# Kernel optimization log

Measured on AMD Instinct MI355X. Metric: run time of the kernel, lower is better.

## Reference

```python
import jax, jax.numpy as jnp
import numpy as np
import math

B, N, DIM, H = 4, 2048, 1024, 16
DH = DIM // H

def setup_inputs() -> dict:
    key = jax.random.key(0)
    ks = jax.random.split(key, 7)
    return {
        "x": jax.random.normal(ks[0], (B, N, DIM), dtype=jnp.float32),
        "qkv_w": jax.random.normal(ks[1], (3 * DIM, DIM), dtype=jnp.float32) * 0.02,
        "qkv_b": jax.random.normal(ks[2], (3 * DIM,), dtype=jnp.float32) * 0.02,
        "proj_w": jax.random.normal(ks[3], (DIM, DIM), dtype=jnp.float32) * 0.02,
        "proj_b": jax.random.normal(ks[4], (DIM,), dtype=jnp.float32) * 0.02,
        "temperature": jnp.ones((1,), dtype=jnp.float32) * 0.1,
        "eps": jax.random.normal(ks[5], (B, H, N, DH), dtype=jnp.float32),
    }

def reference(x, qkv_w, qkv_b, proj_w, proj_b, temperature, eps):
    b, n, dim = x.shape
    qkv = x @ qkv_w.T + qkv_b
    qkv = qkv.reshape(b, n, 3, H, DH).transpose(2, 0, 3, 1, 4)
    q, k, v = qkv[0], qkv[1], qkv[2]
    # quantum fluctuation: additive gaussian noise on q, scaled by sigmoid(temperature)
    q = q + eps * jax.nn.sigmoid(temperature)
    scale = 1.0 / math.sqrt(DH)
    attn = jnp.einsum("bhqd,bhkd->bhqk", q, k) * scale  # [B,H,N,N]
    attn = jax.nn.softmax(attn, axis=-1)
    out = jnp.einsum("bhqk,bhkd->bhqd", attn, v)  # [B,H,N,DH]
    out = out.transpose(0, 2, 1, 3).reshape(b, n, dim)
    return out @ proj_w.T + proj_b
```

## Files before the change

kernel.cpp:

```cpp
#include <hip/hip_runtime.h>
#include <math.h>

#define B_   4
#define N_   2048
#define DIM_ 1024
#define H_   16
#define DH_  64
#define M_   (B_ * N_)
#define QKV_ELEMS ((size_t)B_ * H_ * N_ * DH_)

typedef __attribute__((ext_vector_type(8))) short short8;
typedef __attribute__((ext_vector_type(4))) float floatx4;

static __device__ inline unsigned short f2bf(float f) {
    union { float f; unsigned u; } v; v.f = f;
    unsigned r = (v.u + 0x7fffu + ((v.u >> 16) & 1u)) >> 16;
    return (unsigned short)r;
}

static __device__ inline void async_copy16(const void* g, void* l) {
    __builtin_amdgcn_global_load_lds(
        (const __attribute__((address_space(1))) unsigned int*)g,
        (__attribute__((address_space(3))) unsigned int*)l, 16, 0, 0);
}

__global__ __launch_bounds__(256) void f32_to_bf16_kernel(
    const float* __restrict__ src, unsigned short* __restrict__ dst, int n8)
{
    int i = blockIdx.x * 256 + threadIdx.x;
    if (i >= n8) return;
    float4 a = ((const float4*)src)[i * 2];
    float4 b = ((const float4*)src)[i * 2 + 1];
    short8 o;
    o[0] = f2bf(a.x); o[1] = f2bf(a.y); o[2] = f2bf(a.z); o[3] = f2bf(a.w);
    o[4] = f2bf(b.x); o[5] = f2bf(b.y); o[6] = f2bf(b.z); o[7] = f2bf(b.w);
    *(short8*)(dst + (size_t)i * 8) = o;
}

#define GEMM_BODY(Aptr, Bptr, K)                                               \
    __shared__ unsigned short As[128 * 32];                                    \
    __shared__ unsigned short Bs[128 * 32];                                    \
    const int tid  = threadIdx.x;                                              \
    const int lane = tid & 63;                                                 \
    const int wv   = tid >> 6;                                                 \
    const int l15  = lane & 15, quad = lane >> 4;                              \
    const int wrow = (wv >> 1) * 64, wcol = (wv & 1) * 64;                     \
    const int m0 = blockIdx.y * 128, n0 = blockIdx.x * 128;                    \
    const int lrow = lane >> 2;                                                \
    const int lkc  = (lane & 3) * 8;                                           \
    const unsigned short* ga0 = Aptr + (size_t)(m0 + wv * 32 + lrow) * K + lkc;\
    const unsigned short* ga1 = ga0 + (size_t)16 * K;                          \
    const unsigned short* gb0 = Bptr + (size_t)(n0 + wv * 32 + lrow) * K + lkc;\
    const unsigned short* gb1 = gb0 + (size_t)16 * K;                          \
    unsigned short* lA0 = &As[wv * 1024];                                      \
    unsigned short* lA1 = lA0 + 512;                                           \
    unsigned short* lB0 = &Bs[wv * 1024];                                      \
    unsigned short* lB1 = lB0 + 512;                                           \
    floatx4 acc[4][4] = {};                                                    \
    for (int k0 = 0; k0 < K; k0 += 32) {                                       \
        __syncthreads();                                                       \
        async_copy16(ga0 + k0, lA0);                                           \
        async_copy16(ga1 + k0, lA1);                                           \
        async_copy16(gb0 + k0, lB0);                                           \
        async_copy16(gb1 + k0, lB1);                                           \
        __syncthreads();                                                       \
        short8 af[4], bf[4];                                                   \
        _Pragma("unroll")                                                      \
        for (int mt = 0; mt < 4; ++mt)                                         \
            af[mt] = *(const short8*)&As[(wrow + mt * 16 + l15) * 32 + quad * 8];\
        _Pragma("unroll")                                                      \
        for (int nt = 0; nt < 4; ++nt)                                         \
            bf[nt] = *(const short8*)&Bs[(wcol + nt * 16 + l15) * 32 + quad * 8];\
        _Pragma("unroll")                                                      \
        for (int mt = 0; mt < 4; ++mt)                                         \
            _Pragma("unroll")                                                  \
            for (int nt = 0; nt < 4; ++nt)                                     \
                acc[mt][nt] = __builtin_amdgcn_mfma_f32_16x16x32_bf16(         \
                    af[mt], bf[nt], acc[mt][nt], 0, 0, 0);                     \
    }

__global__ __launch_bounds__(256) void gemm_qkv_bf16(
    const unsigned short* __restrict__ A, const unsigned short* __restrict__ Bm,
    const float* __restrict__ bias, const float* __restrict__ eps,
    const float* __restrict__ temp,
    unsigned short* __restrict__ qb, unsigned short* __restrict__ kb,
    unsigned short* __restrict__ vb)
{
    GEMM_BODY(A, Bm, 1024)

    const float sig = 1.0f / (1.0f + __expf(-temp[0]));
    const float qscale = 0.125f * 1.44269504f;
#pragma unroll
    for (int mt = 0; mt < 4; ++mt) {
#pragma unroll
        for (int r = 0; r < 4; ++r) {
            const int m  = m0 + wrow + mt * 16 + quad * 4 + r;
            const int b  = m >> 11;
            const int nn = m & 2047;
#pragma unroll
            for (int nt = 0; nt < 4; ++nt) {
                const int n = n0 + wcol + nt * 16 + l15;
                float val = acc[mt][nt][r] + bias[n];
                const int which = n >> 10;
                const int d  = n & 1023;
                const int h  = d >> 6;
                const int dd = d & 63;
                const size_t bh = (size_t)(b * H_ + h);
                if (which == 0) {
                    const size_t idx = (bh * N_ + nn) * DH_ + dd;
                    qb[idx] = f2bf((val + eps[idx] * sig) * qscale);
                } else if (which == 1) {
                    kb[(bh * N_ + nn) * DH_ + dd] = f2bf(val);
                } else {
                    vb[(bh * DH_ + dd) * N_ + nn] = f2bf(val);
                }
            }
        }
    }
}

__global__ __launch_bounds__(256) void gemm_proj_bf16(
    const unsigned short* __restrict__ A, const unsigned short* __restrict__ Bm,
    const float* __restrict__ bias, float* __restrict__ out)
{
    GEMM_BODY(A, Bm, 1024)

#pragma unroll
    for (int mt = 0; mt < 4; ++mt) {
#pragma unroll
        for (int r = 0; r < 4; ++r) {
            const int m = m0 + wrow + mt * 16 + quad * 4 + r;
#pragma unroll
            for (int nt = 0; nt < 4; ++nt) {
                const int n = n0 + wcol + nt * 16 + l15;
                out[(size_t)m * 1024 + n] = acc[mt][nt][r] + bias[n];
            }
        }
    }
}

__global__ __launch_bounds__(256) void attn_kernel(
    const unsigned short* __restrict__ qb, const unsigned short* __restrict__ kb,
    const unsigned short* __restrict__ vt, unsigned short* __restrict__ attn_out)
{
    __shared__ unsigned short Ks[64 * 72];
    __shared__ unsigned short Vs[64 * 72];
    __shared__ unsigned short Ps[64 * 72];

    const int tid  = threadIdx.x;
    const int lane = tid & 63;
    const int wv   = tid >> 6;
    const int l15  = lane & 15;
    const int quad = lane >> 4;

    const int bh = blockIdx.y;
    const int b  = bh >> 4, h = bh & 15;
    const int q0 = blockIdx.x * 64;
    const int qr = q0 + wv * 16;

    const unsigned short* qp = qb + ((size_t)bh * N_ + qr + l15) * DH_;
    const short8 qf0 = *(const short8*)(qp + quad * 8);
    const short8 qf1 = *(const short8*)(qp + 32 + quad * 8);

    floatx4 o[4] = {};
    float l_acc[4] = {0.f, 0.f, 0.f, 0.f};

    const unsigned short* kb_bh = kb + (size_t)bh * N_ * DH_;
    const unsigned short* vt_bh = vt + (size_t)bh * DH_ * N_;

    for (int kt = 0; kt < 32; ++kt) {
        const unsigned short* kbase = kb_bh + (size_t)kt * 64 * DH_;
        const unsigned short* vbase = vt_bh + kt * 64;

        __syncthreads();
#pragma unroll
        for (int c = tid; c < 512; c += 256) {
            int r = c >> 3, off = (c & 7) << 3;
            *(short8*)&Ks[r * 72 + off] = *(const short8*)(kbase + r * 64 + off);
            *(short8*)&Vs[r * 72 + off] = *(const short8*)(vbase + (size_t)r * N_ + off);
        }
        __syncthreads();

        floatx4 s[4];
#pragma unroll
        for (int nt = 0; nt < 4; ++nt) {
            const unsigned short* krow = &Ks[(nt * 16 + l15) * 72];
            short8 kf0 = *(const short8*)(krow + quad * 8);
            short8 kf1 = *(const short8*)(krow + 32 + quad * 8);
            floatx4 c = {};
            c = __builtin_amdgcn_mfma_f32_16x16x32_bf16(qf0, kf0, c, 0, 0, 0);
            c = __builtin_amdgcn_mfma_f32_16x16x32_bf16(qf1, kf1, c, 0, 0, 0);
            s[nt] = c;
        }

#pragma unroll
        for (int nt = 0; nt < 4; ++nt)
#pragma unroll
            for (int r = 0; r < 4; ++r)
                s[nt][r] = __builtin_amdgcn_exp2f(s[nt][r]);
#pragma unroll
        for (int r = 0; r < 4; ++r)
            l_acc[r] += (s[0][r] + s[1][r]) + (s[2][r] + s[3][r]);

#pragma unroll
        for (int nt = 0; nt < 4; ++nt)
#pragma unroll
            for (int r = 0; r < 4; ++r) {
                unsigned u = (__float_as_uint(s[nt][r]) + 0x8000u) >> 16;
                Ps[(wv * 16 + quad * 4 + r) * 72 + nt * 16 + l15] = (unsigned short)u;
            }

        const unsigned short* prow = &Ps[(wv * 16 + l15) * 72];
        short8 pf0 = *(const short8*)(prow + quad * 8);
        short8 pf1 = *(const short8*)(prow + 32 + quad * 8);

#pragma unroll
        for (int dt = 0; dt < 4; ++dt) {
            const unsigned short* vrow = &Vs[(dt * 16 + l15) * 72];
            short8 vf0 = *(const short8*)(vrow + quad * 8);
            short8 vf1 = *(const short8*)(vrow + 32 + quad * 8);
            o[dt] = __builtin_amdgcn_mfma_f32_16x16x32_bf16(pf0, vf0, o[dt], 0, 0, 0);
            o[dt] = __builtin_amdgcn_mfma_f32_16x16x32_bf16(pf1, vf1, o[dt], 0, 0, 0);
        }
    }

    float inv[4];
#pragma unroll
    for (int r = 0; r < 4; ++r) {
        float l = l_acc[r];
#pragma unroll
        for (int off = 1; off < 16; off <<= 1)
            l += __shfl_xor(l, off, 64);
        inv[r] = 1.0f / l;
    }

#pragma unroll
    for (int dt = 0; dt < 4; ++dt) {
#pragma unroll
        for (int r = 0; r < 4; ++r) {
            int m = qr + quad * 4 + r;
            attn_out[((size_t)b * N_ + m) * DIM_ + h * DH_ + dt * 16 + l15] =
                f2bf(o[dt][r] * inv[r]);
        }
    }
}

extern "C" void kernel_launch(void* const* d_in, const int* in_sizes, int n_in,
                              void* d_out, int out_size, void* d_ws, size_t ws_size,
                              hipStream_t stream) {
    const float* x      = (const float*)d_in[0];
    const float* qkv_w  = (const float*)d_in[1];
    const float* qkv_b  = (const float*)d_in[2];
    const float* proj_w = (const float*)d_in[3];
    const float* proj_b = (const float*)d_in[4];
    const float* temp   = (const float*)d_in[5];
    const float* eps    = (const float*)d_in[6];
    float* out = (float*)d_out;

    unsigned short* qb   = (unsigned short*)d_ws;
    unsigned short* kb   = qb + QKV_ELEMS;
    unsigned short* vb   = kb + QKV_ELEMS;
    unsigned short* xb   = vb + QKV_ELEMS;
    unsigned short* wqb  = xb + QKV_ELEMS;
    unsigned short* pwb  = wqb + (size_t)3 * DIM_ * DIM_;
    unsigned short* attn = pwb + (size_t)DIM_ * DIM_;

    dim3 blk(256);
    f32_to_bf16_kernel<<<dim3(8388608 / 8 / 256), blk, 0, stream>>>(x, xb, 8388608 / 8);
    f32_to_bf16_kernel<<<dim3(3145728 / 8 / 256), blk, 0, stream>>>(qkv_w, wqb, 3145728 / 8);
    f32_to_bf16_kernel<<<dim3(1048576 / 8 / 256), blk, 0, stream>>>(proj_w, pwb, 1048576 / 8);

    gemm_qkv_bf16<<<dim3(24, 64), blk, 0, stream>>>(xb, wqb, qkv_b, eps, temp,
                                                    qb, kb, vb);
    attn_kernel<<<dim3(32, 64), blk, 0, stream>>>(qb, kb, vb, attn);
    gemm_proj_bf16<<<dim3(8, 64), blk, 0, stream>>>(attn, pwb, proj_b, out);
}
```

Baseline: 390.5 us.

## Restructure attention kernel with async double-buffered K/V, swizzled LDS, 2-wave blocks

Rewrites the attention kernel to use 128-thread blocks where each wave handles 32 query rows, with K/V tiles of 32 keys loaded via async global-to-LDS copies into double buffers so the next tile loads during compute. LDS layouts use XOR swizzles instead of padding, S is computed transposed (K as A operand) so P can be packed and written as bf16 pairs, and s_setprio brackets the MFMA sections. Block indices are remapped so that neighbouring blocks in launch order work on different heads, which is meant to change L2 locality. The aim is to hide global load latency and cut LDS traffic and syncs, at the cost of more registers per wave and more complex indexing.

```diff
diff --git a/kernel.cpp b/kernel.cpp
--- a/kernel.cpp
+++ b/kernel.cpp
@@ -139,108 +139,134 @@
     }
 }
 
-__global__ __launch_bounds__(256) void attn_kernel(
+__global__ __launch_bounds__(128) void attn_kernel(
     const unsigned short* __restrict__ qb, const unsigned short* __restrict__ kb,
     const unsigned short* __restrict__ vt, unsigned short* __restrict__ attn_out)
 {
-    __shared__ unsigned short Ks[64 * 72];
-    __shared__ unsigned short Vs[64 * 72];
-    __shared__ unsigned short Ps[64 * 72];
+    __shared__ unsigned short Ks[2][32 * 64];
+    __shared__ unsigned short Vs[2][64 * 32];
+    __shared__ unsigned short Ps[64 * 40];
 
     const int tid  = threadIdx.x;
     const int lane = tid & 63;
     const int wv   = tid >> 6;
     const int l15  = lane & 15;
     const int quad = lane >> 4;
-
-    const int bh = blockIdx.y;
+    const int s7   = l15 & 7;
+    const int s3   = l15 & 3;
+
+    const int f  = blockIdx.y * 32 + blockIdx.x;
+    const int L  = (f & 7) * 256 + (f >> 3);
+    const int bh = L >> 5;
     const int b  = bh >> 4, h = bh & 15;
-    const int q0 = blockIdx.x * 64;
-    const int qr = q0 + wv * 16;
-
-    const unsigned short* qp = qb + ((size_t)bh * N_ + qr + l15) * DH_;
-    const short8 qf0 = *(const short8*)(qp + quad * 8);
-    const short8 qf1 = *(const short8*)(qp + 32 + quad * 8);
-
-    floatx4 o[4] = {};
-    float l_acc[4] = {0.f, 0.f, 0.f, 0.f};
+    const int q0 = (L & 31) * 64;
 
     const unsigned short* kb_bh = kb + (size_t)bh * N_ * DH_;
     const unsigned short* vt_bh = vt + (size_t)bh * DH_ * N_;
 
-    for (int kt = 0; kt < 32; ++kt) {
-        const unsigned short* kbase = kb_bh + (size_t)kt * 64 * DH_;
-        const unsigned short* vbase = vt_bh + kt * 64;
-
+    short8 qf[2][2];
+#pragma unroll
+    for (int g = 0; g < 2; ++g) {
+        const unsigned short* qp =
+            qb + ((size_t)bh * N_ + q0 + wv * 32 + g * 16 + l15) * DH_;
+        qf[g][0] = *(const short8*)(qp + quad * 8);
+        qf[g][1] = *(const short8*)(qp + 32 + quad * 8);
+    }
+
+    floatx4 o[2][4] = {};
+    float l_part[2] = {0.f, 0.f};
+
+    const int kr  = tid >> 3;
+    const int kls = (tid & 7) ^ (kr & 7);
+    const int vd  = tid >> 2;
+    const int vls = (tid & 3) ^ (vd & 3);
+
+#define STAGE(buf, kt)                                                           \
+    do {                                                                         \
+        _Pragma("unroll")                                                        \
+        for (int c = 0; c < 2; ++c) {                                            \
+            async_copy16(kb_bh + (size_t)((kt) * 32 + c * 16 + kr) * DH_ + kls * 8, \
+                         &Ks[buf][c * 1024 + wv * 512]);                         \
+            async_copy16(vt_bh + (size_t)(c * 32 + vd) * N_ + (kt) * 32 + vls * 8,  \
+                         &Vs[buf][c * 1024 + wv * 512]);                         \
+        }                                                                        \
+    } while (0)
+
+    STAGE(0, 0);
+
+#pragma unroll 2
+    for (int kt = 0; kt < 64; ++kt) {
+        const int cur = kt & 1;
         __syncthreads();
-#pragma unroll
-        for (int c = tid; c < 512; c += 256) {
-            int r = c >> 3, off = (c & 7) << 3;
-            *(short8*)&Ks[r * 72 + off] = *(const short8*)(kbase + r * 64 + off);
-            *(short8*)&Vs[r * 72 + off] = *(const short8*)(vbase + (size_t)r * N_ + off);
-        }
-        __syncthreads();
-
-        floatx4 s[4];
-#pragma unroll
-        for (int nt = 0; nt < 4; ++nt) {
-            const unsigned short* krow = &Ks[(nt * 16 + l15) * 72];
-            short8 kf0 = *(const short8*)(krow + quad * 8);
-            short8 kf1 = *(const short8*)(krow + 32 + quad * 8);
-            floatx4 c = {};
-            c = __builtin_amdgcn_mfma_f32_16x16x32_bf16(qf0, kf0, c, 0, 0, 0);
-            c = __builtin_amdgcn_mfma_f32_16x16x32_bf16(qf1, kf1, c, 0, 0, 0);
-            s[nt] = c;
-        }
-
-#pragma unroll
-        for (int nt = 0; nt < 4; ++nt)
-#pragma unroll
-            for (int r = 0; r < 4; ++r)
-                s[nt][r] = __builtin_amdgcn_exp2f(s[nt][r]);
-#pragma unroll
-        for (int r = 0; r < 4; ++r)
-            l_acc[r] += (s[0][r] + s[1][r]) + (s[2][r] + s[3][r]);
-
-#pragma unroll
-        for (int nt = 0; nt < 4; ++nt)
-#pragma unroll
-            for (int r = 0; r < 4; ++r) {
-                unsigned u = (__float_as_uint(s[nt][r]) + 0x8000u) >> 16;
-                Ps[(wv * 16 + quad * 4 + r) * 72 + nt * 16 + l15] = (unsigned short)u;
+        if (kt < 63) STAGE(cur ^ 1, kt + 1);
+
+        const unsigned short* Kc = Ks[cur];
+        const unsigned short* Vc = Vs[cur];
+
+        short8 kf[2][2];
+#pragma unroll
+        for (int nt = 0; nt < 2; ++nt) {
+            const int off0 = (nt * 16 + l15) * 64 + (quad ^ s7) * 8;
+            kf[nt][0] = *(const short8*)(Kc + off0);
+            kf[nt][1] = *(const short8*)(Kc + (off0 ^ 32));
+        }
+        short8 vf[4];
+#pragma unroll
+        for (int dt = 0; dt < 4; ++dt)
+            vf[dt] = *(const short8*)(Vc + (dt * 16 + l15) * 32 + (quad ^ s3) * 8);
+
+#pragma unroll
+        for (int g = 0; g < 2; ++g) {
+            const int prow = wv * 32 + g * 16 + l15;
+            floatx4 s[2];
+            __builtin_amdgcn_s_setprio(1);
+#pragma unroll
+            for (int nt = 0; nt < 2; ++nt) {
+                floatx4 c = {};
+                c = __builtin_amdgcn_mfma_f32_16x16x32_bf16(kf[nt][0], qf[g][0], c, 0, 0, 0);
+                c = __builtin_amdgcn_mfma_f32_16x16x32_bf16(kf[nt][1], qf[g][1], c, 0, 0, 0);
+                s[nt] = c;
             }
-
-        const unsigned short* prow = &Ps[(wv * 16 + l15) * 72];
-        short8 pf0 = *(const short8*)(prow + quad * 8);
-        short8 pf1 = *(const short8*)(prow + 32 + quad * 8);
-
-#pragma unroll
-        for (int dt = 0; dt < 4; ++dt) {
-            const unsigned short* vrow = &Vs[(dt * 16 + l15) * 72];
-            short8 vf0 = *(const short8*)(vrow + quad * 8);
-            short8 vf1 = *(const short8*)(vrow + 32 + quad * 8);
-            o[dt] = __builtin_amdgcn_mfma_f32_16x16x32_bf16(pf0, vf0, o[dt], 0, 0, 0);
-            o[dt] = __builtin_amdgcn_mfma_f32_16x16x32_bf16(pf1, vf1, o[dt], 0, 0, 0);
-        }
-    }
-
-    float inv[4];
-#pragma unroll
-    for (int r = 0; r < 4; ++r) {
-        float l = l_acc[r];
-#pragma unroll
-        for (int off = 1; off < 16; off <<= 1)
-            l += __shfl_xor(l, off, 64);
-        inv[r] = 1.0f / l;
-    }
-
-#pragma unroll
-    for (int dt = 0; dt < 4; ++dt) {
+            __builtin_amdgcn_s_setprio(0);
+
+#pragma unroll
+            for (int nt = 0; nt < 2; ++nt) {
+#pragma unroll
+                for (int r = 0; r < 4; ++r)
+                    s[nt][r] = __builtin_amdgcn_exp2f(s[nt][r]);
+                l_part[g] += (s[nt][0] + s[nt][1]) + (s[nt][2] + s[nt][3]);
+                unsigned w0 = ((__float_as_uint(s[nt][0]) + 0x8000u) >> 16) |
+                              ((__float_as_uint(s[nt][1]) + 0x8000u) & 0xffff0000u);
+                unsigned w1 = ((__float_as_uint(s[nt][2]) + 0x8000u) >> 16) |
+                              ((__float_as_uint(s[nt][3]) + 0x8000u) & 0xffff0000u);
+                uint2 wp; wp.x = w0; wp.y = w1;
+                *(uint2*)&Ps[prow * 40 + nt * 16 + quad * 4] = wp;
+            }
+            const short8 pf = *(const short8*)&Ps[prow * 40 + quad * 8];
+
+            __builtin_amdgcn_s_setprio(1);
+#pragma unroll
+            for (int dt = 0; dt < 4; ++dt)
+                o[g][dt] = __builtin_amdgcn_mfma_f32_16x16x32_bf16(pf, vf[dt], o[g][dt], 0, 0, 0);
+            __builtin_amdgcn_s_setprio(0);
+        }
+    }
+#undef STAGE
+
+#pragma unroll
+    for (int g = 0; g < 2; ++g) {
+        float lsum = l_part[g];
+        lsum += __shfl_xor(lsum, 16, 64);
+        lsum += __shfl_xor(lsum, 32, 64);
+        const float inv = 1.0f / lsum;
 #pragma unroll
         for (int r = 0; r < 4; ++r) {
-            int m = qr + quad * 4 + r;
-            attn_out[((size_t)b * N_ + m) * DIM_ + h * DH_ + dt * 16 + l15] =
-                f2bf(o[dt][r] * inv[r]);
+            const float invq = __shfl(inv, quad * 4 + r, 64);
+            const int row = q0 + wv * 32 + g * 16 + quad * 4 + r;
+#pragma unroll
+            for (int dt = 0; dt < 4; ++dt)
+                attn_out[((size_t)b * N_ + row) * DIM_ + h * DH_ + dt * 16 + l15] =
+                    f2bf(o[g][dt][r] * invq);
         }
     }
 }
@@ -272,6 +298,6 @@
 
     gemm_qkv_bf16<<<dim3(24, 64), blk, 0, stream>>>(xb, wqb, qkv_b, eps, temp,
                                                     qb, kb, vb);
-    attn_kernel<<<dim3(32, 64), blk, 0, stream>>>(qb, kb, vb, attn);
+    attn_kernel<<<dim3(32, 64), dim3(128), 0, stream>>>(qb, kb, vb, attn);
     gemm_proj_bf16<<<dim3(8, 64), blk, 0, stream>>>(attn, pwb, proj_b, out);
 }
```

Result: slower. 399.6 us (+2.3%).

## Restructure attention to LDS-free register tiles with transposed S and shuffled P

Applied to the files above, without the earlier changes.

Rewrites the attention kernel so each wave owns 64 query rows and computes S transposed (K as the A operand), loading K and V fragments directly from global memory into registers with double-buffered K prefetch. This removes all shared memory and __syncthreads. P is rearranged into the MFMA operand layout with cross-lane shuffles instead of a round trip through LDS. The grid becomes 1D with a swizzle for L2 locality, plus launch bounds of 2 and s_setprio around the MFMAs. The cost is heavier register use and redundant global/L2 reads of K and V across waves.

```diff
diff --git a/kernel.cpp b/kernel.cpp
--- a/kernel.cpp
+++ b/kernel.cpp
@@ -16,6 +16,12 @@
     union { float f; unsigned u; } v; v.f = f;
     unsigned r = (v.u + 0x7fffu + ((v.u >> 16) & 1u)) >> 16;
     return (unsigned short)r;
+}
+
+static __device__ inline unsigned pkbf(float a, float b) {
+    unsigned ua = (__float_as_uint(a) + 0x8000u) >> 16;
+    unsigned ub = (__float_as_uint(b) + 0x8000u) & 0xffff0000u;
+    return ua | ub;
 }
 
 static __device__ inline void async_copy16(const void* g, void* l) {
@@ -139,108 +145,128 @@
     }
 }
 
-__global__ __launch_bounds__(256) void attn_kernel(
+__global__ __launch_bounds__(256, 2) void attn_kernel(
     const unsigned short* __restrict__ qb, const unsigned short* __restrict__ kb,
     const unsigned short* __restrict__ vt, unsigned short* __restrict__ attn_out)
 {
-    __shared__ unsigned short Ks[64 * 72];
-    __shared__ unsigned short Vs[64 * 72];
-    __shared__ unsigned short Ps[64 * 72];
-
     const int tid  = threadIdx.x;
     const int lane = tid & 63;
     const int wv   = tid >> 6;
     const int l15  = lane & 15;
     const int quad = lane >> 4;
-
-    const int bh = blockIdx.y;
+    const int q1   = quad >> 1;
+    const int q0b  = quad & 1;
+
+    const int f  = blockIdx.x;
+    const int L  = (f & 7) * 64 + (f >> 3);
+    const int bh = L >> 3;
     const int b  = bh >> 4, h = bh & 15;
-    const int q0 = blockIdx.x * 64;
-    const int qr = q0 + wv * 16;
-
-    const unsigned short* qp = qb + ((size_t)bh * N_ + qr + l15) * DH_;
-    const short8 qf0 = *(const short8*)(qp + quad * 8);
-    const short8 qf1 = *(const short8*)(qp + 32 + quad * 8);
-
-    floatx4 o[4] = {};
-    float l_acc[4] = {0.f, 0.f, 0.f, 0.f};
+    const int qbase = (L & 7) * 256 + wv * 64;
 
     const unsigned short* kb_bh = kb + (size_t)bh * N_ * DH_;
     const unsigned short* vt_bh = vt + (size_t)bh * DH_ * N_;
 
-    for (int kt = 0; kt < 32; ++kt) {
-        const unsigned short* kbase = kb_bh + (size_t)kt * 64 * DH_;
-        const unsigned short* vbase = vt_bh + kt * 64;
-
-        __syncthreads();
-#pragma unroll
-        for (int c = tid; c < 512; c += 256) {
-            int r = c >> 3, off = (c & 7) << 3;
-            *(short8*)&Ks[r * 72 + off] = *(const short8*)(kbase + r * 64 + off);
-            *(short8*)&Vs[r * 72 + off] = *(const short8*)(vbase + (size_t)r * N_ + off);
-        }
-        __syncthreads();
-
-        floatx4 s[4];
-#pragma unroll
-        for (int nt = 0; nt < 4; ++nt) {
-            const unsigned short* krow = &Ks[(nt * 16 + l15) * 72];
-            short8 kf0 = *(const short8*)(krow + quad * 8);
-            short8 kf1 = *(const short8*)(krow + 32 + quad * 8);
-            floatx4 c = {};
-            c = __builtin_amdgcn_mfma_f32_16x16x32_bf16(qf0, kf0, c, 0, 0, 0);
-            c = __builtin_amdgcn_mfma_f32_16x16x32_bf16(qf1, kf1, c, 0, 0, 0);
-            s[nt] = c;
-        }
-
-#pragma unroll
-        for (int nt = 0; nt < 4; ++nt)
-#pragma unroll
-            for (int r = 0; r < 4; ++r)
-                s[nt][r] = __builtin_amdgcn_exp2f(s[nt][r]);
-#pragma unroll
-        for (int r = 0; r < 4; ++r)
-            l_acc[r] += (s[0][r] + s[1][r]) + (s[2][r] + s[3][r]);
-
-#pragma unroll
-        for (int nt = 0; nt < 4; ++nt)
-#pragma unroll
-            for (int r = 0; r < 4; ++r) {
-                unsigned u = (__float_as_uint(s[nt][r]) + 0x8000u) >> 16;
-                Ps[(wv * 16 + quad * 4 + r) * 72 + nt * 16 + l15] = (unsigned short)u;
-            }
-
-        const unsigned short* prow = &Ps[(wv * 16 + l15) * 72];
-        short8 pf0 = *(const short8*)(prow + quad * 8);
-        short8 pf1 = *(const short8*)(prow + 32 + quad * 8);
-
-#pragma unroll
-        for (int dt = 0; dt < 4; ++dt) {
-            const unsigned short* vrow = &Vs[(dt * 16 + l15) * 72];
-            short8 vf0 = *(const short8*)(vrow + quad * 8);
-            short8 vf1 = *(const short8*)(vrow + 32 + quad * 8);
-            o[dt] = __builtin_amdgcn_mfma_f32_16x16x32_bf16(pf0, vf0, o[dt], 0, 0, 0);
-            o[dt] = __builtin_amdgcn_mfma_f32_16x16x32_bf16(pf1, vf1, o[dt], 0, 0, 0);
-        }
-    }
-
-    float inv[4];
-#pragma unroll
-    for (int r = 0; r < 4; ++r) {
-        float l = l_acc[r];
-#pragma unroll
-        for (int off = 1; off < 16; off <<= 1)
-            l += __shfl_xor(l, off, 64);
-        inv[r] = 1.0f / l;
-    }
-
-#pragma unroll
-    for (int dt = 0; dt < 4; ++dt) {
+    short8 qf[4][2];
+#pragma unroll
+    for (int g = 0; g < 4; ++g) {
+        const unsigned short* qp =
+            qb + ((size_t)bh * N_ + qbase + g * 16 + l15) * DH_;
+        qf[g][0] = *(const short8*)(qp + quad * 8);
+        qf[g][1] = *(const short8*)(qp + 32 + quad * 8);
+    }
+
+    floatx4 o[4][4] = {};
+    float l_part[4] = {0.f, 0.f, 0.f, 0.f};
+
+    const unsigned short* kA = kb_bh + (size_t)l15 * DH_ + quad * 8;
+    const unsigned short* vA = vt_bh + (size_t)l15 * N_ + quad * 8;
+
+    short8 kfA[2][2], kfB[2][2];
+
+#define LOADK(DST, ktn)                                                        \
+    do {                                                                       \
+        _Pragma("unroll")                                                      \
+        for (int nt = 0; nt < 2; ++nt) {                                       \
+            _Pragma("unroll")                                                  \
+            for (int hh = 0; hh < 2; ++hh)                                     \
+                DST[nt][hh] = *(const short8*)(                                \
+                    kA + (size_t)((ktn) * 32 + nt * 16) * DH_ + hh * 32);      \
+        }                                                                      \
+    } while (0)
+
+#define TILE(CUR, NXT, kt, ktn)                                                \
+    do {                                                                       \
+        short8 vf[4];                                                          \
+        _Pragma("unroll")                                                      \
+        for (int dt = 0; dt < 4; ++dt)                                         \
+            vf[dt] = *(const short8*)(vA + (size_t)dt * 16 * N_ + (kt) * 32);  \
+        LOADK(NXT, ktn);                             \
+        _Pragma("unroll")                                                      \
+        for (int g = 0; g < 4; ++g) {                                          \
+            floatx4 s0 = {}, s1 = {};                                          \
+            __builtin_amdgcn_s_setprio(1);                                     \
+            s0 = __builtin_amdgcn_mfma_f32_16x16x32_bf16(CUR[0][0], qf[g][0], s0, 0, 0, 0); \
+            s0 = __builtin_amdgcn_mfma_f32_16x16x32_bf16(CUR[0][1], qf[g][1], s0, 0, 0, 0); \
+            s1 = __builtin_amdgcn_mfma_f32_16x16x32_bf16(CUR[1][0], qf[g][0], s1, 0, 0, 0); \
+            s1 = __builtin_amdgcn_mfma_f32_16x16x32_bf16(CUR[1][1], qf[g][1], s1, 0, 0, 0); \
+            __builtin_amdgcn_s_setprio(0);                                     \
+            _Pragma("unroll")                                                  \
+            for (int r = 0; r < 4; ++r) {                                      \
+                s0[r] = __builtin_amdgcn_exp2f(s0[r]);                         \
+                s1[r] = __builtin_amdgcn_exp2f(s1[r]);                         \
+            }                                                                  \
+            l_part[g] += ((s0[0] + s0[1]) + (s0[2] + s0[3]))                   \
+                       + ((s1[0] + s1[1]) + (s1[2] + s1[3]));                  \
+                           \
+            unsigned w0 = pkbf(s0[0], s0[1]);                                  \
+            unsigned w1 = pkbf(s0[2], s0[3]);                                  \
+            unsigned w2 = pkbf(s1[0], s1[1]);                                  \
+            unsigned w3 = pkbf(s1[2], s1[3]);                                  \
+                  \
+            unsigned t0 = q1 ? w0 : w2, t1 = q1 ? w1 : w3;                     \
+            unsigned r0 = (unsigned)__shfl_xor((int)t0, 32, 64);               \
+            unsigned r1 = (unsigned)__shfl_xor((int)t1, 32, 64);               \
+            unsigned m0 = q1 ? r0 : w0, m1 = q1 ? r1 : w1;                     \
+            unsigned m2 = q1 ? w2 : r0, m3 = q1 ? w3 : r1;                     \
+                  \
+            unsigned u0 = q0b ? m0 : m2, u1 = q0b ? m1 : m3;                   \
+            unsigned x0 = (unsigned)__shfl_xor((int)u0, 16, 64);               \
+            unsigned x1 = (unsigned)__shfl_xor((int)u1, 16, 64);               \
+            union { unsigned u[4]; short8 s8; } pu;                            \
+            pu.u[0] = q0b ? x0 : m0; pu.u[1] = q0b ? x1 : m1;                  \
+            pu.u[2] = q0b ? m2 : x0; pu.u[3] = q0b ? m3 : x1;                  \
+            const short8 pf = pu.s8;    \
+            __builtin_amdgcn_s_setprio(1);                                     \
+            _Pragma("unroll")                                                  \
+            for (int dt = 0; dt < 4; ++dt)                                     \
+                o[g][dt] = __builtin_amdgcn_mfma_f32_16x16x32_bf16(            \
+                    pf, vf[dt], o[g][dt], 0, 0, 0);                            \
+            __builtin_amdgcn_s_setprio(0);                                     \
+        }                                                                      \
+    } while (0)
+
+    LOADK(kfA, 0);
+    for (int kt = 0; kt < 64; kt += 2) {
+        TILE(kfA, kfB, kt, kt + 1);
+        TILE(kfB, kfA, kt + 1, (kt + 2 < 64) ? (kt + 2) : 0);
+    }
+#undef TILE
+#undef LOADK
+
+#pragma unroll
+    for (int g = 0; g < 4; ++g) {
+        float lsum = l_part[g];
+        lsum += __shfl_xor(lsum, 16, 64);
+        lsum += __shfl_xor(lsum, 32, 64);
+        const float inv = 1.0f / lsum;
 #pragma unroll
         for (int r = 0; r < 4; ++r) {
-            int m = qr + quad * 4 + r;
-            attn_out[((size_t)b * N_ + m) * DIM_ + h * DH_ + dt * 16 + l15] =
-                f2bf(o[dt][r] * inv[r]);
+            const float invq = __shfl(inv, quad * 4 + r, 64);
+            const int row = qbase + g * 16 + quad * 4 + r;
+#pragma unroll
+            for (int dt = 0; dt < 4; ++dt)
+                attn_out[((size_t)b * N_ + row) * DIM_ + h * DH_ + dt * 16 + l15] =
+                    f2bf(o[g][dt][r] * invq);
         }
     }
 }
@@ -272,6 +298,6 @@
 
     gemm_qkv_bf16<<<dim3(24, 64), blk, 0, stream>>>(xb, wqb, qkv_b, eps, temp,
                                                     qb, kb, vb);
-    attn_kernel<<<dim3(32, 64), blk, 0, stream>>>(qb, kb, vb, attn);
+    attn_kernel<<<dim3(512), dim3(256), 0, stream>>>(qb, kb, vb, attn);
     gemm_proj_bf16<<<dim3(8, 64), blk, 0, stream>>>(attn, pwb, proj_b, out);
 }
```

Result: no change. 395.5 us (+1.3%).
